# Kernel tuning notes

Measured on AMD Instinct MI355X. Metric: run time of the kernel, lower is better.

Reference implementation:

```python
import jax, jax.numpy as jnp
import numpy as np

NUM_HEADS = 8


def setup_inputs() -> dict:
    key = jax.random.key(0)
    k1, k2, k3 = jax.random.split(key, 3)
    B, N, C = 4, 2048, 768
    x = jax.random.normal(k1, (B, N, C), dtype=jnp.float32)
    proj_w = jax.random.normal(k2, (C, C), dtype=jnp.float32) * (C ** -0.5)
    proj_b = jax.random.normal(k3, (C,), dtype=jnp.float32) * 0.01
    return {"x": x, "proj_w": proj_w, "proj_b": proj_b}


def reference(x, proj_w, proj_b):
    B, N, C = x.shape
    H = NUM_HEADS
    d = C // H
    scale = d ** -0.5
    # NOTE: original forward ignores the qkv Linear; q = k = v = reshaped x.
    qkv = x.reshape(B, N, H, d).transpose(0, 2, 1, 3)  # (B, H, N, d)
    attn = jnp.einsum('bhnd,bhmd->bhnm', qkv, qkv) * scale  # (B, H, N, N)
    attn = jax.nn.softmax(attn, axis=-1)
    out = jnp.einsum('bhnm,bhmd->bhnd', attn, qkv)  # (B, H, N, d)
    out = out.transpose(0, 2, 1, 3).reshape(B, N, C)
    # nn.Linear: y = out @ W^T + b
    return out @ proj_w.T + proj_b
```

## Files before the change

kernel.cpp:

```cpp
#include <hip/hip_runtime.h>
#include <hip/hip_bf16.h>

#define B_ 4
#define N_ 2048
#define C_ 768
#define H_ 8
#define D_ 96

typedef __attribute__((ext_vector_type(8))) short bf16x8;
typedef __attribute__((ext_vector_type(4))) float f32x4;

static __device__ __forceinline__ unsigned short bf16b(float f) {
  __hip_bfloat16 h = __float2bfloat16(f);
  return __builtin_bit_cast(unsigned short, h);
}

__global__ __launch_bounds__(64) void k_prep(const float* __restrict__ x,
                                             __hip_bfloat16* __restrict__ Xbf,
                                             __hip_bfloat16* __restrict__ Vtg) {
  const int t = threadIdx.x;
  const int nc = blockIdx.x, bh = blockIdx.y;
  const int b = bh >> 3, h = bh & 7;
  const int n = nc * 64 + t;
  const size_t rowoff = ((size_t)(b * N_ + n)) * C_ + h * D_;
  const float* src = x + rowoff;
  __hip_bfloat16* dx = Xbf + rowoff;
#pragma unroll
  for (int c8 = 0; c8 < 12; ++c8) {
    float4 lo = *(const float4*)(src + c8 * 8);
    float4 hi = *(const float4*)(src + c8 * 8 + 4);
    unsigned short u0 = bf16b(lo.x), u1 = bf16b(lo.y), u2 = bf16b(lo.z), u3 = bf16b(lo.w);
    unsigned short u4 = bf16b(hi.x), u5 = bf16b(hi.y), u6 = bf16b(hi.z), u7 = bf16b(hi.w);
    uint4 pk;
    pk.x = (unsigned)u0 | ((unsigned)u1 << 16);
    pk.y = (unsigned)u2 | ((unsigned)u3 << 16);
    pk.z = (unsigned)u4 | ((unsigned)u5 << 16);
    pk.w = (unsigned)u6 | ((unsigned)u7 << 16);
    *(uint4*)(dx + c8 * 8) = pk;
    unsigned short uu[8] = {u0, u1, u2, u3, u4, u5, u6, u7};
#pragma unroll
    for (int e = 0; e < 8; ++e) {
      __hip_bfloat16 hv = __builtin_bit_cast(__hip_bfloat16, uu[e]);
      Vtg[((size_t)(bh * D_ + c8 * 8 + e)) * N_ + n] = hv;
    }
  }
}

__global__ __launch_bounds__(256) void k_castw(const float* __restrict__ w,
                                               __hip_bfloat16* __restrict__ Wbf) {
  const int i = blockIdx.x * 256 + threadIdx.x;
  float4 f = *(const float4*)(w + (size_t)i * 4);
  unsigned v0 = (unsigned)bf16b(f.x) | ((unsigned)bf16b(f.y) << 16);
  unsigned v1 = (unsigned)bf16b(f.z) | ((unsigned)bf16b(f.w) << 16);
  uint2 pk; pk.x = v0; pk.y = v1;
  *(uint2*)(Wbf + (size_t)i * 4) = pk;
}

static __device__ __forceinline__ bf16x8 scale8(bf16x8 v, float s) {
  bf16x8 r;
#pragma unroll
  for (int e = 0; e < 8; ++e) {
    __hip_bfloat16 hv = __builtin_bit_cast(__hip_bfloat16, (unsigned short)v[e]);
    r[e] = (short)bf16b(__bfloat162float(hv) * s);
  }
  return r;
}

__global__ __launch_bounds__(512, 4) void k_attn(const __hip_bfloat16* __restrict__ Xbf,
                                                 const __hip_bfloat16* __restrict__ Vtg,
                                                 __hip_bfloat16* __restrict__ Ybf) {
  __shared__ __hip_bfloat16 K2[2][64][104];
  __shared__ __hip_bfloat16 V2[2][96][72];
  __shared__ __hip_bfloat16 Plds[8][16][72];

  const int tid = threadIdx.x;
  const int wid = tid >> 6, lane = tid & 63;
  const int lr = lane & 15, lg = lane >> 4;
  const int qt = blockIdx.x, bh = blockIdx.y;
  const int b = bh >> 3, h = bh & 7;
  const int q0 = qt * 128 + wid * 16;
  const float SL2E = 0.14724444f;

  bf16x8 qf[3];
  {
    const __hip_bfloat16* qp = Xbf + ((size_t)(b * N_ + q0 + lr)) * C_ + h * D_ + lg * 8;
    qf[0] = scale8(*(const bf16x8*)(qp), SL2E);
    qf[1] = scale8(*(const bf16x8*)(qp + 32), SL2E);
    qf[2] = scale8(*(const bf16x8*)(qp + 64), SL2E);
  }

  const __hip_bfloat16* Kbase = Xbf + ((size_t)b * N_) * C_ + h * D_;
  const __hip_bfloat16* Vbase = Vtg + ((size_t)bh * D_) * N_;

  bf16x8 sreg[3];
  auto stage_load = [&](int kv0) {
#pragma unroll
    for (int i = 0; i < 3; ++i) {
      int idx = tid + i * 512;
      if (idx < 768) {
        int r = idx / 12, c = idx - r * 12;
        sreg[i] = *(const bf16x8*)(Kbase + (size_t)(kv0 + r) * C_ + c * 8);
      } else {
        int j = idx - 768;
        int r = j >> 3, c = j & 7;
        sreg[i] = *(const bf16x8*)(Vbase + (size_t)r * N_ + kv0 + c * 8);
      }
    }
  };
  auto stage_write = [&](int buf) {
#pragma unroll
    for (int i = 0; i < 3; ++i) {
      int idx = tid + i * 512;
      if (idx < 768) {
        int r = idx / 12, c = idx - r * 12;
        *(bf16x8*)(&K2[buf][r][c * 8]) = sreg[i];
      } else {
        int j = idx - 768;
        int r = j >> 3, c = j & 7;
        *(bf16x8*)(&V2[buf][r][c * 8]) = sreg[i];
      }
    }
  };

  const f32x4 fzero = {0.f, 0.f, 0.f, 0.f};
  f32x4 accO[6];
#pragma unroll
  for (int ct = 0; ct < 6; ++ct) accO[ct] = fzero;
  float lrun = 0.f;

  stage_load(0);
  stage_write(0);
  __syncthreads();

  int cur = 0;
  for (int kv0 = 0; kv0 < N_; kv0 += 64) {
    const int nxt = kv0 + 64;
    if (nxt < N_) stage_load(nxt);

    f32x4 accS[4];
#pragma unroll
    for (int tk = 0; tk < 4; ++tk) {
      accS[tk] = fzero;
#pragma unroll
      for (int kk = 0; kk < 3; ++kk) {
        bf16x8 kf = *(const bf16x8*)(&K2[cur][tk * 16 + lr][kk * 32 + lg * 8]);
        accS[tk] = __builtin_amdgcn_mfma_f32_16x16x32_bf16(kf, qf[kk], accS[tk], 0, 0, 0);
      }
    }

    float tv[16];
    float psum = 0.f;
#pragma unroll
    for (int tk = 0; tk < 4; ++tk)
#pragma unroll
      for (int j = 0; j < 4; ++j) {
        float v = exp2f(accS[tk][j]);
        tv[tk * 4 + j] = v;
        psum += v;
      }
    psum += __shfl_xor(psum, 16);
    psum += __shfl_xor(psum, 32);
    lrun += psum;
#pragma unroll
    for (int tk = 0; tk < 4; ++tk) {
      ushort4 pk;
      pk.x = bf16b(tv[tk * 4 + 0]);
      pk.y = bf16b(tv[tk * 4 + 1]);
      pk.z = bf16b(tv[tk * 4 + 2]);
      pk.w = bf16b(tv[tk * 4 + 3]);
      *(ushort4*)(&Plds[wid][lr][tk * 16 + lg * 4]) = pk;
    }

    bf16x8 pa[2];
#pragma unroll
    for (int ks = 0; ks < 2; ++ks)
      pa[ks] = *(const bf16x8*)(&Plds[wid][lr][ks * 32 + lg * 8]);
#pragma unroll
    for (int ks = 0; ks < 2; ++ks) {
#pragma unroll
      for (int ct = 0; ct < 6; ++ct) {
        bf16x8 vb = *(const bf16x8*)(&V2[cur][ct * 16 + lr][ks * 32 + lg * 8]);
        accO[ct] = __builtin_amdgcn_mfma_f32_16x16x32_bf16(pa[ks], vb, accO[ct], 0, 0, 0);
      }
    }

    if (nxt < N_) stage_write(cur ^ 1);
    __syncthreads();
    cur ^= 1;
  }

  float linv[4];
#pragma unroll
  for (int j = 0; j < 4; ++j) linv[j] = 1.0f / __shfl(lrun, lg * 4 + j);
  __hip_bfloat16* yb = Ybf + ((size_t)(b * N_ + q0 + lg * 4)) * C_ + h * D_ + lr;
#pragma unroll
  for (int ct = 0; ct < 6; ++ct)
#pragma unroll
    for (int j = 0; j < 4; ++j)
      yb[(size_t)j * C_ + ct * 16] = __float2bfloat16(accO[ct][j] * linv[j]);
}

__global__ __launch_bounds__(256) void k_proj(const __hip_bfloat16* __restrict__ Ybf,
                                              const __hip_bfloat16* __restrict__ Wbf,
                                              const float* __restrict__ bias,
                                              float* __restrict__ out) {
  __shared__ __hip_bfloat16 Alds[128][40];
  __shared__ __hip_bfloat16 Blds[128][40];
  const int tid = threadIdx.x, wid = tid >> 6, lane = tid & 63;
  const int lr = lane & 15, lg = lane >> 4;
  const int m0 = blockIdx.x * 128, n0 = blockIdx.y * 128;
  const int wm = (wid >> 1) * 64, wn = (wid & 1) * 64;

  const f32x4 fzero = {0.f, 0.f, 0.f, 0.f};
  f32x4 acc[4][4];
#pragma unroll
  for (int mi = 0; mi < 4; ++mi)
#pragma unroll
    for (int ni = 0; ni < 4; ++ni) acc[mi][ni] = fzero;

  for (int k0 = 0; k0 < C_; k0 += 32) {
#pragma unroll
    for (int i = 0; i < 2; ++i) {
      int idx = tid + i * 256;
      int r = idx >> 2, cc = idx & 3;
      *(bf16x8*)(&Alds[r][cc * 8]) =
          *(const bf16x8*)(Ybf + (size_t)(m0 + r) * C_ + k0 + cc * 8);
      *(bf16x8*)(&Blds[r][cc * 8]) =
          *(const bf16x8*)(Wbf + (size_t)(n0 + r) * C_ + k0 + cc * 8);
    }
    __syncthreads();
    bf16x8 af[4], bfr[4];
#pragma unroll
    for (int i = 0; i < 4; ++i) {
      af[i] = *(const bf16x8*)(&Alds[wm + i * 16 + lr][lg * 8]);
      bfr[i] = *(const bf16x8*)(&Blds[wn + i * 16 + lr][lg * 8]);
    }
#pragma unroll
    for (int mi = 0; mi < 4; ++mi)
#pragma unroll
      for (int ni = 0; ni < 4; ++ni)
        acc[mi][ni] = __builtin_amdgcn_mfma_f32_16x16x32_bf16(af[mi], bfr[ni], acc[mi][ni], 0, 0, 0);
    __syncthreads();
  }

#pragma unroll
  for (int mi = 0; mi < 4; ++mi) {
#pragma unroll
    for (int ni = 0; ni < 4; ++ni) {
      int col = n0 + wn + ni * 16 + lr;
      float bv = bias[col];
#pragma unroll
      for (int j = 0; j < 4; ++j) {
        int row = m0 + wm + mi * 16 + lg * 4 + j;
        out[(size_t)row * C_ + col] = acc[mi][ni][j] + bv;
      }
    }
  }
}

extern "C" void kernel_launch(void* const* d_in, const int* in_sizes, int n_in,
                              void* d_out, int out_size, void* d_ws, size_t ws_size,
                              hipStream_t stream) {
  const float* x = (const float*)d_in[0];
  const float* pw = (const float*)d_in[1];
  const float* pb = (const float*)d_in[2];
  float* out = (float*)d_out;

  __hip_bfloat16* Xbf = (__hip_bfloat16*)d_ws;
  __hip_bfloat16* Vtg = Xbf + (size_t)B_ * N_ * C_;
  __hip_bfloat16* Wbf = Vtg + (size_t)B_ * N_ * C_;
  __hip_bfloat16* Ybf = Wbf + (size_t)C_ * C_;

  k_prep<<<dim3(N_ / 64, B_ * H_), 64, 0, stream>>>(x, Xbf, Vtg);
  k_castw<<<(C_ * C_ / 4) / 256, 256, 0, stream>>>(pw, Wbf);
  k_attn<<<dim3(N_ / 128, B_ * H_), 512, 0, stream>>>(Xbf, Vtg, Ybf);
  k_proj<<<dim3((B_ * N_) / 128, C_ / 128), 256, 0, stream>>>(Ybf, Wbf, pb, out);
}
```

Baseline: 125.3 us.

## Switch attention to 32x32x16 MFMA with in-register P via permlane32 swap

Rewrites the attention kernel so each wave handles 32 query rows with 32x32x16 bf16 MFMAs instead of 16 rows with 16x16x32, halving the block to 256 threads. The softmax probabilities are repacked to bf16 in registers using v_permlane32_swap rather than a round trip through a per-wave LDS buffer. The global K/V prefetch now issues after the QK^T MFMAs, with precomputed pointers and LDS offsets. This should cut LDS traffic and address math per tile, at the cost of more registers per thread and fewer waves per block.

Result: no change. 124.4 us (-0.7%).

```diff
diff --git a/kernel.cpp b/kernel.cpp
--- a/kernel.cpp
+++ b/kernel.cpp
@@ -9,10 +9,15 @@
 
 typedef __attribute__((ext_vector_type(8))) short bf16x8;
 typedef __attribute__((ext_vector_type(4))) float f32x4;
+typedef __attribute__((ext_vector_type(16))) float f32x16;
+typedef __attribute__((ext_vector_type(4))) unsigned u32x4;
 
 static __device__ __forceinline__ unsigned short bf16b(float f) {
   __hip_bfloat16 h = __float2bfloat16(f);
   return __builtin_bit_cast(unsigned short, h);
+}
+static __device__ __forceinline__ unsigned pack2(float a, float b) {
+  return (unsigned)bf16b(a) | ((unsigned)bf16b(b) << 16);
 }
 
 __global__ __launch_bounds__(64) void k_prep(const float* __restrict__ x,
@@ -66,138 +71,147 @@
   return r;
 }
 
-__global__ __launch_bounds__(512, 4) void k_attn(const __hip_bfloat16* __restrict__ Xbf,
+__global__ __launch_bounds__(256, 3) void k_attn(const __hip_bfloat16* __restrict__ Xbf,
                                                  const __hip_bfloat16* __restrict__ Vtg,
                                                  __hip_bfloat16* __restrict__ Ybf) {
   __shared__ __hip_bfloat16 K2[2][64][104];
   __shared__ __hip_bfloat16 V2[2][96][72];
-  __shared__ __hip_bfloat16 Plds[8][16][72];
 
   const int tid = threadIdx.x;
   const int wid = tid >> 6, lane = tid & 63;
-  const int lr = lane & 15, lg = lane >> 4;
+  const int lr = lane & 31, hi = lane >> 5;
   const int qt = blockIdx.x, bh = blockIdx.y;
   const int b = bh >> 3, h = bh & 7;
-  const int q0 = qt * 128 + wid * 16;
+  const int q0w = qt * 128 + wid * 32;
   const float SL2E = 0.14724444f;
 
-  bf16x8 qf[3];
+  bf16x8 qf[6];
   {
-    const __hip_bfloat16* qp = Xbf + ((size_t)(b * N_ + q0 + lr)) * C_ + h * D_ + lg * 8;
-    qf[0] = scale8(*(const bf16x8*)(qp), SL2E);
-    qf[1] = scale8(*(const bf16x8*)(qp + 32), SL2E);
-    qf[2] = scale8(*(const bf16x8*)(qp + 64), SL2E);
+    const __hip_bfloat16* qp =
+        Xbf + ((size_t)(b * N_ + q0w + lr)) * C_ + h * D_ + hi * 8;
+#pragma unroll
+    for (int kk = 0; kk < 6; ++kk)
+      qf[kk] = scale8(*(const bf16x8*)(qp + kk * 16), SL2E);
   }
 
   const __hip_bfloat16* Kbase = Xbf + ((size_t)b * N_) * C_ + h * D_;
   const __hip_bfloat16* Vbase = Vtg + ((size_t)bh * D_) * N_;
 
-  bf16x8 sreg[3];
-  auto stage_load = [&](int kv0) {
-#pragma unroll
-    for (int i = 0; i < 3; ++i) {
-      int idx = tid + i * 512;
-      if (idx < 768) {
-        int r = idx / 12, c = idx - r * 12;
-        sreg[i] = *(const bf16x8*)(Kbase + (size_t)(kv0 + r) * C_ + c * 8);
-      } else {
-        int j = idx - 768;
-        int r = j >> 3, c = j & 7;
-        sreg[i] = *(const bf16x8*)(Vbase + (size_t)r * N_ + kv0 + c * 8);
-      }
+  const __hip_bfloat16* gp[6];
+  int lofs[6];
+#pragma unroll
+  for (int i = 0; i < 6; ++i) {
+    if (i < 3) {
+      int idx = tid + i * 256;
+      int r = idx / 12, c = idx - r * 12;
+      gp[i] = Kbase + (size_t)r * C_ + c * 8;
+      lofs[i] = r * 104 + c * 8;
+    } else {
+      int j = tid + (i - 3) * 256;
+      int r = j >> 3, c = j & 7;
+      gp[i] = Vbase + (size_t)r * N_ + c * 8;
+      lofs[i] = r * 72 + c * 8;
+    }
+  }
+  bf16x8 sreg[6];
+  auto stage_load = [&]() {
+#pragma unroll
+    for (int i = 0; i < 6; ++i) {
+      sreg[i] = *(const bf16x8*)gp[i];
+      gp[i] += (i < 3) ? 64 * C_ : 64;
     }
   };
   auto stage_write = [&](int buf) {
 #pragma unroll
-    for (int i = 0; i < 3; ++i) {
-      int idx = tid + i * 512;
-      if (idx < 768) {
-        int r = idx / 12, c = idx - r * 12;
-        *(bf16x8*)(&K2[buf][r][c * 8]) = sreg[i];
-      } else {
-        int j = idx - 768;
-        int r = j >> 3, c = j & 7;
-        *(bf16x8*)(&V2[buf][r][c * 8]) = sreg[i];
-      }
+    for (int i = 0; i < 6; ++i) {
+      if (i < 3)
+        *(bf16x8*)(&K2[buf][0][0] + lofs[i]) = sreg[i];
+      else
+        *(bf16x8*)(&V2[buf][0][0] + lofs[i]) = sreg[i];
     }
   };
 
-  const f32x4 fzero = {0.f, 0.f, 0.f, 0.f};
-  f32x4 accO[6];
-#pragma unroll
-  for (int ct = 0; ct < 6; ++ct) accO[ct] = fzero;
+  f32x16 accO[3] = {};
   float lrun = 0.f;
 
-  stage_load(0);
+  stage_load();
   stage_write(0);
   __syncthreads();
 
   int cur = 0;
   for (int kv0 = 0; kv0 < N_; kv0 += 64) {
-    const int nxt = kv0 + 64;
-    if (nxt < N_) stage_load(nxt);
-
-    f32x4 accS[4];
-#pragma unroll
-    for (int tk = 0; tk < 4; ++tk) {
-      accS[tk] = fzero;
-#pragma unroll
-      for (int kk = 0; kk < 3; ++kk) {
-        bf16x8 kf = *(const bf16x8*)(&K2[cur][tk * 16 + lr][kk * 32 + lg * 8]);
-        accS[tk] = __builtin_amdgcn_mfma_f32_16x16x32_bf16(kf, qf[kk], accS[tk], 0, 0, 0);
-      }
-    }
-
-    float tv[16];
+    const bool more = (kv0 + 64) < N_;
+
+    f32x16 accS[2] = {};
+#pragma unroll
+    for (int kk = 0; kk < 6; ++kk) {
+#pragma unroll
+      for (int tk = 0; tk < 2; ++tk) {
+        bf16x8 kf = *(const bf16x8*)(&K2[cur][tk * 32 + lr][kk * 16 + hi * 8]);
+        accS[tk] = __builtin_amdgcn_mfma_f32_32x32x16_bf16(kf, qf[kk], accS[tk], 0, 0, 0);
+      }
+    }
+
+    if (more) stage_load();
+
     float psum = 0.f;
 #pragma unroll
-    for (int tk = 0; tk < 4; ++tk)
-#pragma unroll
-      for (int j = 0; j < 4; ++j) {
-        float v = exp2f(accS[tk][j]);
-        tv[tk * 4 + j] = v;
+    for (int tk = 0; tk < 2; ++tk)
+#pragma unroll
+      for (int r = 0; r < 16; ++r) {
+        float v = exp2f(accS[tk][r]);
+        accS[tk][r] = v;
         psum += v;
       }
-    psum += __shfl_xor(psum, 16);
-    psum += __shfl_xor(psum, 32);
     lrun += psum;
-#pragma unroll
-    for (int tk = 0; tk < 4; ++tk) {
-      ushort4 pk;
-      pk.x = bf16b(tv[tk * 4 + 0]);
-      pk.y = bf16b(tv[tk * 4 + 1]);
-      pk.z = bf16b(tv[tk * 4 + 2]);
-      pk.w = bf16b(tv[tk * 4 + 3]);
-      *(ushort4*)(&Plds[wid][lr][tk * 16 + lg * 4]) = pk;
-    }
-
-    bf16x8 pa[2];
-#pragma unroll
-    for (int ks = 0; ks < 2; ++ks)
-      pa[ks] = *(const bf16x8*)(&Plds[wid][lr][ks * 32 + lg * 8]);
-#pragma unroll
-    for (int ks = 0; ks < 2; ++ks) {
-#pragma unroll
-      for (int ct = 0; ct < 6; ++ct) {
-        bf16x8 vb = *(const bf16x8*)(&V2[cur][ct * 16 + lr][ks * 32 + lg * 8]);
-        accO[ct] = __builtin_amdgcn_mfma_f32_16x16x32_bf16(pa[ks], vb, accO[ct], 0, 0, 0);
-      }
-    }
-
-    if (nxt < N_) stage_write(cur ^ 1);
+
+    bf16x8 pbf[4];
+#pragma unroll
+    for (int tk = 0; tk < 2; ++tk) {
+#pragma unroll
+      for (int s = 0; s < 2; ++s) {
+        unsigned lo0 = pack2(accS[tk][8 * s + 0], accS[tk][8 * s + 1]);
+        unsigned lo1 = pack2(accS[tk][8 * s + 2], accS[tk][8 * s + 3]);
+        unsigned hi0 = pack2(accS[tk][8 * s + 4], accS[tk][8 * s + 5]);
+        unsigned hi1 = pack2(accS[tk][8 * s + 6], accS[tk][8 * s + 7]);
+        asm volatile("v_permlane32_swap_b32 %0, %1" : "+v"(lo0), "+v"(hi0));
+        asm volatile("v_permlane32_swap_b32 %0, %1" : "+v"(lo1), "+v"(hi1));
+        u32x4 pw;
+        pw.x = lo0; pw.y = lo1; pw.z = hi0; pw.w = hi1;
+        pbf[tk * 2 + s] = __builtin_bit_cast(bf16x8, pw);
+      }
+    }
+
+#pragma unroll
+    for (int ks = 0; ks < 4; ++ks) {
+#pragma unroll
+      for (int dt = 0; dt < 3; ++dt) {
+        bf16x8 va = *(const bf16x8*)(&V2[cur][dt * 32 + lr][ks * 16 + hi * 8]);
+        accO[dt] = __builtin_amdgcn_mfma_f32_32x32x16_bf16(va, pbf[ks], accO[dt], 0, 0, 0);
+      }
+    }
+
+    if (more) stage_write(cur ^ 1);
     __syncthreads();
     cur ^= 1;
   }
 
-  float linv[4];
-#pragma unroll
-  for (int j = 0; j < 4; ++j) linv[j] = 1.0f / __shfl(lrun, lg * 4 + j);
-  __hip_bfloat16* yb = Ybf + ((size_t)(b * N_ + q0 + lg * 4)) * C_ + h * D_ + lr;
-#pragma unroll
-  for (int ct = 0; ct < 6; ++ct)
-#pragma unroll
-    for (int j = 0; j < 4; ++j)
-      yb[(size_t)j * C_ + ct * 16] = __float2bfloat16(accO[ct][j] * linv[j]);
+  float ltot = lrun + __shfl_xor(lrun, 32);
+  float linv = 1.0f / ltot;
+  __hip_bfloat16* yb =
+      Ybf + ((size_t)(b * N_ + q0w + lr)) * C_ + h * D_ + hi * 4;
+#pragma unroll
+  for (int dt = 0; dt < 3; ++dt) {
+#pragma unroll
+    for (int rq = 0; rq < 4; ++rq) {
+      ushort4 pk;
+      pk.x = bf16b(accO[dt][rq * 4 + 0] * linv);
+      pk.y = bf16b(accO[dt][rq * 4 + 1] * linv);
+      pk.z = bf16b(accO[dt][rq * 4 + 2] * linv);
+      pk.w = bf16b(accO[dt][rq * 4 + 3] * linv);
+      *(ushort4*)(yb + dt * 32 + rq * 8) = pk;
+    }
+  }
 }
 
 __global__ __launch_bounds__(256) void k_proj(const __hip_bfloat16* __restrict__ Ybf,
@@ -273,6 +287,6 @@
 
   k_prep<<<dim3(N_ / 64, B_ * H_), 64, 0, stream>>>(x, Xbf, Vtg);
   k_castw<<<(C_ * C_ / 4) / 256, 256, 0, stream>>>(pw, Wbf);
-  k_attn<<<dim3(N_ / 128, B_ * H_), 512, 0, stream>>>(Xbf, Vtg, Ybf);
+  k_attn<<<dim3(N_ / 128, B_ * H_), 256, 0, stream>>>(Xbf, Vtg, Ybf);
   k_proj<<<dim3((B_ * N_) / 128, C_ / 128), 256, 0, stream>>>(Ybf, Wbf, pb, out);
 }
```
